# Optimization experiments

Hardware: AMD Instinct MI355X
Metric: run time of the kernel (lower is better)

The kernel has to match this reference:

```python
import jax, jax.numpy as jnp
import numpy as np

B, S, D, H = 4, 2048, 1024, 16
DH = D // H  # 64


def setup_inputs() -> dict:
    key = jax.random.key(0)
    ks = jax.random.split(key, 9)
    scale = 1.0 / np.sqrt(D)
    x = jax.random.normal(ks[0], (B, S, D), dtype=jnp.float32)
    # Stacked per-head projection weights, equivalent to ModuleList of Linear(D, DH)
    Wq = jax.random.uniform(ks[1], (H, D, DH), jnp.float32, -scale, scale)
    bq = jax.random.uniform(ks[2], (H, DH), jnp.float32, -scale, scale)
    Wk = jax.random.uniform(ks[3], (H, D, DH), jnp.float32, -scale, scale)
    bk = jax.random.uniform(ks[4], (H, DH), jnp.float32, -scale, scale)
    Wv = jax.random.uniform(ks[5], (H, D, DH), jnp.float32, -scale, scale)
    bv = jax.random.uniform(ks[6], (H, DH), jnp.float32, -scale, scale)
    Wo = jax.random.uniform(ks[7], (D, D), jnp.float32, -scale, scale)
    bo = jax.random.uniform(ks[8], (D,), jnp.float32, -scale, scale)
    return {"x": x, "Wq": Wq, "bq": bq, "Wk": Wk, "bk": bk,
            "Wv": Wv, "bv": bv, "Wo": Wo, "bo": bo}


def reference(x, Wq, bq, Wk, bk, Wv, bv, Wo, bo):
    # Per-head Linear projections, batched across heads: [B,S,D]x[H,D,DH] -> [B,H,S,DH]
    q = jnp.einsum('bsd,hde->bhse', x, Wq) + bq[None, :, None, :]
    k = jnp.einsum('bsd,hde->bhse', x, Wk) + bk[None, :, None, :]
    v = jnp.einsum('bsd,hde->bhse', x, Wv) + bv[None, :, None, :]
    # Scaled dot-product attention (no mask is applied in the original forward)
    scores = jnp.einsum('bhse,bhte->bhst', q, k) / jnp.sqrt(jnp.float32(DH))
    attn = jax.nn.softmax(scores, axis=-1)
    z = jnp.einsum('bhst,bhte->bhse', attn, v)  # [B,H,S,DH]
    # Concat heads on last dim (head-major order matches torch.cat over dim=-1)
    multihead = jnp.transpose(z, (0, 2, 1, 3)).reshape(B, S, D)
    return multihead @ Wo + bo
```

## Files before the change

### kernel.cpp

```cpp
#include <hip/hip_runtime.h>
#include <hip/hip_bf16.h>
#include <cstdint>
#include <cstddef>


typedef unsigned short u16;
typedef unsigned int u32;
typedef __attribute__((ext_vector_type(8))) __bf16 bf16x8;
typedef __attribute__((ext_vector_type(8))) unsigned short u16x8;
typedef __attribute__((ext_vector_type(4))) float f32x4;
typedef __attribute__((ext_vector_type(4))) unsigned int u32x4;

__device__ __forceinline__ u16 f2bf(float f) {
  union { __hip_bfloat16 h; u16 u; } c;
  c.h = __float2bfloat16(f);
  return c.u;
}
#if defined(__has_builtin)
#if __has_builtin(__builtin_amdgcn_cvt_pk_bf16_f32)
#define HAS_PK_BF16 1
#endif
#endif
__device__ __forceinline__ u32 pk2c(float a, float b) {
#ifdef HAS_PK_BF16
  return __builtin_bit_cast(u32, __builtin_amdgcn_cvt_pk_bf16_f32(a, b));
#else
  const u32 ua = __float_as_uint(a);
  const u32 ub = __float_as_uint(b);
  const u32 ra = ua + 0x7FFFu + ((ua >> 16) & 1u);
  const u32 rb = ub + 0x7FFFu + ((ub >> 16) & 1u);
  return (ra >> 16) | (rb & 0xFFFF0000u);
#endif
}
__device__ __forceinline__ float ex2(float x) {
  return __builtin_amdgcn_exp2f(x);
}

__device__ __forceinline__ void async16(const void* g, void* l) {
  __builtin_amdgcn_global_load_lds(
      (const __attribute__((address_space(1))) void*)g,
      (__attribute__((address_space(3))) void*)l, 16, 0, 0);
}

__global__ void k_pack_all(const float* __restrict__ x,
                           const float* __restrict__ Wq, const float* __restrict__ Wk,
                           const float* __restrict__ Wv,
                           const float* __restrict__ bq, const float* __restrict__ bk,
                           const float* __restrict__ bv,
                           const float* __restrict__ Wo,
                           u16* __restrict__ xb, u16* __restrict__ Wt,
                           float* __restrict__ bqkv, u16* __restrict__ Wot) {
  __shared__ __align__(16) u16 tile[64][72];
  const int bid = blockIdx.x;
  const int t = threadIdx.x;
  if (bid < 1024) {
    const float* src;
    u16* dstp;
    int rstride, n_base, d0;
    if (bid < 768) {
      const int proj = bid >> 8, h = (bid >> 4) & 15, dt = bid & 15;
      const float* Wp = (proj == 0) ? Wq : ((proj == 1) ? Wk : Wv);
      src = Wp + h * 65536 + (dt * 64) * 64;
      rstride = 64;
      n_base = proj * 1024 + h * 64;
      d0 = dt * 64;
      dstp = Wt;
    } else {
      const int tb = bid - 768, nt = tb >> 4, dt = tb & 15;
      src = Wo + (size_t)(dt * 64) * 1024 + nt * 64;
      rstride = 1024;
      n_base = nt * 64;
      d0 = dt * 64;
      dstp = Wot;
    }
    {
      const int row = t >> 2, c0 = (t & 3) * 16;
      const float* s = src + row * rstride + c0;
#pragma unroll
      for (int j = 0; j < 4; ++j) {
        const float4 v = *(const float4*)(s + j * 4);
        ushort4 o;
        o.x = f2bf(v.x); o.y = f2bf(v.y); o.z = f2bf(v.z); o.w = f2bf(v.w);
        *(ushort4*)&tile[row][c0 + j * 4] = o;
      }
    }
    __syncthreads();
    {
      const int e = t >> 2, c0 = (t & 3) * 16;
      u16 buf[16];
#pragma unroll
      for (int i = 0; i < 16; ++i) buf[i] = tile[c0 + i][e];
      u16* d = dstp + (size_t)(n_base + e) * 1024 + d0 + c0;
      *(u16x8*)d = *(const u16x8*)&buf[0];
      *(u16x8*)(d + 8) = *(const u16x8*)&buf[8];
    }
  } else if (bid < 9216) {
    const int i = ((bid - 1024) * 256 + t) * 4;
    const float4 v = *(const float4*)(x + i);
    ushort4 o;
    o.x = f2bf(v.x); o.y = f2bf(v.y); o.z = f2bf(v.z); o.w = f2bf(v.w);
    *(ushort4*)(xb + i) = o;
  } else {
    const int n = (bid - 9216) * 256 + t;
    const int proj = n >> 10, rem = n & 1023, h = rem >> 6, e = rem & 63;
    const float* bp = (proj == 0) ? bq : ((proj == 1) ? bk : bv);
    bqkv[n] = bp[h * 64 + e];
  }
}

template <int MODE>
__global__ __launch_bounds__(256)
void k_gemm(const u16* __restrict__ A, const u16* __restrict__ Bt,
            const float* __restrict__ bias, void* __restrict__ Cout, int ldc) {
  __shared__ __align__(16) u16 Alds[128 * 32];
  __shared__ __align__(16) u16 Blds[128 * 32];
  const int t = threadIdx.x;
  const int lane = t & 63;
  const int w = t >> 6;
  const int l15 = lane & 15;
  const int quad = lane >> 4;
  const int wm = w >> 1, wn = w & 1;
  const int m0 = blockIdx.y << 7;
  const int n0 = blockIdx.x << 7;

  const u16* ga0 = A + (size_t)(m0 + (t >> 2)) * 1024 + (t & 3) * 8;
  const u16* ga1 = ga0 + (size_t)64 * 1024;
  const u16* gb0 = Bt + (size_t)(n0 + (t >> 2)) * 1024 + (t & 3) * 8;
  const u16* gb1 = gb0 + (size_t)64 * 1024;
  u16* const lA0 = Alds + w * 512;
  u16* const lA1 = Alds + w * 512 + 2048;
  u16* const lB0 = Blds + w * 512;
  u16* const lB1 = Blds + w * 512 + 2048;

  f32x4 acc[4][4];
#pragma unroll
  for (int mi = 0; mi < 4; ++mi)
#pragma unroll
    for (int ni = 0; ni < 4; ++ni) acc[mi][ni] = (f32x4){0.f, 0.f, 0.f, 0.f};

  for (int k0 = 0; k0 < 1024; k0 += 32) {
    __syncthreads();
    async16(ga0, lA0); async16(ga1, lA1);
    async16(gb0, lB0); async16(gb1, lB1);
    ga0 += 32; ga1 += 32; gb0 += 32; gb1 += 32;
    __syncthreads();
    bf16x8 af[4], bfr[4];
#pragma unroll
    for (int i = 0; i < 4; ++i) {
      af[i]  = *(const bf16x8*)(Alds + (wm * 64 + i * 16 + l15) * 32 + quad * 8);
      bfr[i] = *(const bf16x8*)(Blds + (wn * 64 + i * 16 + l15) * 32 + quad * 8);
    }
#pragma unroll
    for (int mi = 0; mi < 4; ++mi)
#pragma unroll
      for (int ni = 0; ni < 4; ++ni)
        acc[mi][ni] = __builtin_amdgcn_mfma_f32_16x16x32_bf16(af[mi], bfr[ni], acc[mi][ni], 0, 0, 0);
  }

  const int row0 = m0 + wm * 64;
  const int col0 = n0 + wn * 64;
  const float qscale = (MODE == 0 && col0 < 1024) ? 0.125f * 1.4426950408889634f : 1.0f;
#pragma unroll
  for (int mi = 0; mi < 4; ++mi) {
#pragma unroll
    for (int ni = 0; ni < 4; ++ni) {
      const int col = col0 + ni * 16 + l15;
      const float bb = bias[col];
#pragma unroll
      for (int r = 0; r < 4; ++r) {
        const int row = row0 + mi * 16 + quad * 4 + r;
        const float v = (acc[mi][ni][r] + bb) * qscale;
        if (MODE == 0) ((u16*)Cout)[(size_t)row * ldc + col] = f2bf(v);
        else           ((float*)Cout)[(size_t)row * ldc + col] = v;
      }
    }
  }
}

__global__ __launch_bounds__(256)
void k_vt(const u16* __restrict__ qkv, u16* __restrict__ vtg) {
  __shared__ u16 tile[64][72];
  const int t = threadIdx.x;
  const int bh = blockIdx.y, b = bh >> 4, h = bh & 15;
  const int s0 = blockIdx.x << 6;
  {
    const int row = t >> 2, col0 = (t & 3) * 16;
    const u16* src = qkv + (size_t)(b * 2048 + s0 + row) * 3072 + 2048 + h * 64 + col0;
    const u16x8 v0 = *(const u16x8*)src;
    const u16x8 v1 = *(const u16x8*)(src + 8);
    *(u16x8*)&tile[row][col0] = v0;
    *(u16x8*)&tile[row][col0 + 8] = v1;
  }
  __syncthreads();
  {
    const int e = t >> 2, sc = (t & 3) * 16;
    u16 buf[16];
#pragma unroll
    for (int i = 0; i < 16; ++i) buf[i] = tile[sc + i][e];
    u16* dst = vtg + ((size_t)bh * 64 + e) * 2048 + s0 + sc;
    *(u16x8*)dst = *(const u16x8*)&buf[0];
    *(u16x8*)(dst + 8) = *(const u16x8*)&buf[8];
  }
}

__global__ __launch_bounds__(256)
void k_attn(const u16* __restrict__ qkv, const u16* __restrict__ vtg,
            u16* __restrict__ mh) {
  __shared__ __align__(16) u16 smem[16384];
  u16* const Klds = smem;
  u16* const Vlds = smem + 8192;

  const int t = threadIdx.x;
  const int lane = t & 63;
  const int w = t >> 6;
  const int l15 = lane & 15;
  const int quad = lane >> 4;
  const int bh = blockIdx.x, b = bh >> 4, h = bh & 15;
  const int s0 = blockIdx.y << 7;

  const int lam0 = t >> 3;
  const int key0 = (lam0 & 3) | (((lam0 >> 2) & 3) << 3) | (((lam0 >> 4) & 1) << 2);
  const int ck = (t & 7) ^ (lam0 & 7);
  const u16* kbase = qkv + (size_t)(b * 2048 + key0) * 3072 + 1024 + h * 64 + ck * 8;
  const int e0 = t >> 4;
  const int cv = (t & 15) ^ e0;
  const u16* vbase = vtg + ((size_t)bh * 64 + e0) * 2048 + cv * 8;
  u16* const KldsW = Klds + w * 512;
  u16* const VldsW = Vlds + w * 512;

  bf16x8 aq[2][2];
#pragma unroll
  for (int g = 0; g < 2; ++g)
#pragma unroll
    for (int ks2 = 0; ks2 < 2; ++ks2)
      aq[g][ks2] = *(const bf16x8*)(qkv +
          (size_t)(b * 2048 + s0 + w * 32 + g * 16 + l15) * 3072 +
          h * 64 + ks2 * 32 + quad * 8);

  const u32x4 onesu = (u32x4){0x3F803F80u, 0x3F803F80u, 0x3F803F80u, 0x3F803F80u};
  const bf16x8 ones = __builtin_bit_cast(bf16x8, onesu);

  f32x4 o[2][4];
  f32x4 lacc[2];
#pragma unroll
  for (int g = 0; g < 2; ++g) {
    lacc[g] = (f32x4){0.f, 0.f, 0.f, 0.f};
#pragma unroll
    for (int ne = 0; ne < 4; ++ne) o[g][ne] = (f32x4){0.f, 0.f, 0.f, 0.f};
  }

  for (int kt = 0; kt < 16; ++kt) {
    __syncthreads();
#pragma unroll
    for (int r = 0; r < 4; ++r)
      async16(kbase + r * (32 * 3072), KldsW + r * 2048);
#pragma unroll
    for (int r = 0; r < 4; ++r)
      async16(vbase + r * (16 * 2048), VldsW + r * 2048);
    kbase += 128 * 3072;
    vbase += 128;
    __syncthreads();

#pragma unroll
    for (int ks = 0; ks < 4; ++ks) {
      u32x4 pf[2];
#pragma unroll
      for (int h2 = 0; h2 < 2; ++h2) {
        const int kt8 = ks * 2 + h2;
        const int row = kt8 * 16 + l15;
        const bf16x8 kf0 = *(const bf16x8*)(Klds + row * 64 + ((quad) ^ (l15 & 7)) * 8);
        const bf16x8 kf1 = *(const bf16x8*)(Klds + row * 64 + ((4 + quad) ^ (l15 & 7)) * 8);
        f32x4 st[2];
#pragma unroll
        for (int g = 0; g < 2; ++g) {
          st[g] = __builtin_amdgcn_mfma_f32_16x16x32_bf16(kf0, aq[g][0], (f32x4){0.f,0.f,0.f,0.f}, 0, 0, 0);
          st[g] = __builtin_amdgcn_mfma_f32_16x16x32_bf16(kf1, aq[g][1], st[g], 0, 0, 0);
        }
#pragma unroll
        for (int g = 0; g < 2; ++g) {
          const float p0 = ex2(st[g][0]), p1 = ex2(st[g][1]);
          const float p2 = ex2(st[g][2]), p3 = ex2(st[g][3]);
          pf[g][h2 * 2 + 0] = pk2c(p0, p1);
          pf[g][h2 * 2 + 1] = pk2c(p2, p3);
        }
      }
#pragma unroll
      for (int ne = 0; ne < 4; ++ne) {
        const int e = ne * 16 + l15;
        const bf16x8 bv8 = *(const bf16x8*)(Vlds + e * 128 + (((ks * 4 + quad) ^ l15) & 15) * 8);
#pragma unroll
        for (int g = 0; g < 2; ++g)
          o[g][ne] = __builtin_amdgcn_mfma_f32_16x16x32_bf16(
              __builtin_bit_cast(bf16x8, pf[g]), bv8, o[g][ne], 0, 0, 0);
      }
#pragma unroll
      for (int g = 0; g < 2; ++g)
        lacc[g] = __builtin_amdgcn_mfma_f32_16x16x32_bf16(
            __builtin_bit_cast(bf16x8, pf[g]), ones, lacc[g], 0, 0, 0);
    }
  }

#pragma unroll
  for (int g = 0; g < 2; ++g) {
#pragma unroll
    for (int r = 0; r < 4; ++r) {
      const float iv = 1.f / lacc[g][r];
      const int row = s0 + w * 32 + g * 16 + quad * 4 + r;
#pragma unroll
      for (int ne = 0; ne < 4; ++ne) {
        const int col = h * 64 + ne * 16 + l15;
        mh[(size_t)(b * 2048 + row) * 1024 + col] = f2bf(o[g][ne][r] * iv);
      }
    }
  }
}

extern "C" void kernel_launch(void* const* d_in, const int* in_sizes, int n_in,
                              void* d_out, int out_size, void* d_ws, size_t ws_size,
                              hipStream_t stream) {
  (void)in_sizes; (void)n_in; (void)out_size; (void)ws_size;
  const float* x  = (const float*)d_in[0];
  const float* Wq = (const float*)d_in[1];
  const float* bq = (const float*)d_in[2];
  const float* Wk = (const float*)d_in[3];
  const float* bk = (const float*)d_in[4];
  const float* Wv = (const float*)d_in[5];
  const float* bv = (const float*)d_in[6];
  const float* Wo = (const float*)d_in[7];
  const float* bo = (const float*)d_in[8];

  char* ws = (char*)d_ws;
  u16*   Xb   = (u16*)  (ws + 0);
  u16*   Vtg  = (u16*)  (ws + 0);
  u16*   Wt   = (u16*)  (ws + 16777216);
  float* bqkv = (float*)(ws + 23068672);
  u16*   Wot  = (u16*)  (ws + 23080960);
  u16*   QKV  = (u16*)  (ws + 25178112);
  u16*   MH   = (u16*)  (ws + 75509760);
  float* out  = (float*)d_out;

  k_pack_all <<<9228, 256, 0, stream>>>(x, Wq, Wk, Wv, bq, bk, bv, Wo,
                                        Xb, Wt, bqkv, Wot);
  k_gemm<0>  <<<dim3(24, 64), 256, 0, stream>>>(Xb, Wt, bqkv, (void*)QKV, 3072);
  k_vt       <<<dim3(32, 64), 256, 0, stream>>>(QKV, Vtg);
  k_attn     <<<dim3(64, 16), 256, 0, stream>>>(QKV, Vtg, MH);
  k_gemm<1>  <<<dim3(8, 64), 256, 0, stream>>>(MH, Wot, bo, (void*)out, 1024);
}
```

Baseline: 295.5 us.

## Double-buffer K/V tiles in LDS with async prefetch and MFMA priority hints

Splits the 128-key tile into 64-key tiles and alternates between two LDS buffers, so the next tile's asynchronous global-to-LDS loads are issued before the current tile is computed. A partial vmcnt wait and raw barriers replace the full syncthreads pair. s_setprio is raised around MFMA blocks to favour matrix issue across waves. The V LDS layout and swizzle are changed to match the 64-key stride. The tradeoff is more barriers per key and reliance on the vmcnt count being correct.

```diff
diff --git a/kernel.cpp b/kernel.cpp
--- a/kernel.cpp
+++ b/kernel.cpp
@@ -207,8 +207,6 @@
 void k_attn(const u16* __restrict__ qkv, const u16* __restrict__ vtg,
             u16* __restrict__ mh) {
   __shared__ __align__(16) u16 smem[16384];
-  u16* const Klds = smem;
-  u16* const Vlds = smem + 8192;
 
   const int t = threadIdx.x;
   const int lane = t & 63;
@@ -222,11 +220,12 @@
   const int key0 = (lam0 & 3) | (((lam0 >> 2) & 3) << 3) | (((lam0 >> 4) & 1) << 2);
   const int ck = (t & 7) ^ (lam0 & 7);
   const u16* kbase = qkv + (size_t)(b * 2048 + key0) * 3072 + 1024 + h * 64 + ck * 8;
-  const int e0 = t >> 4;
-  const int cv = (t & 15) ^ e0;
+  const int e0 = t >> 3;
+  const int cv = (t & 7) ^ (e0 & 7);
   const u16* vbase = vtg + ((size_t)bh * 64 + e0) * 2048 + cv * 8;
-  u16* const KldsW = Klds + w * 512;
-  u16* const VldsW = Vlds + w * 512;
+
+  const int kofs = w * 512;
+  const int vofs = 4096 + w * 512;
 
   bf16x8 aq[2][2];
 #pragma unroll
@@ -249,33 +248,49 @@
     for (int ne = 0; ne < 4; ++ne) o[g][ne] = (f32x4){0.f, 0.f, 0.f, 0.f};
   }
 
-  for (int kt = 0; kt < 16; ++kt) {
-    __syncthreads();
-#pragma unroll
-    for (int r = 0; r < 4; ++r)
-      async16(kbase + r * (32 * 3072), KldsW + r * 2048);
-#pragma unroll
-    for (int r = 0; r < 4; ++r)
-      async16(vbase + r * (16 * 2048), VldsW + r * 2048);
-    kbase += 128 * 3072;
-    vbase += 128;
-    __syncthreads();
-
-#pragma unroll
-    for (int ks = 0; ks < 4; ++ks) {
+#pragma unroll
+  for (int r = 0; r < 2; ++r) {
+    async16(kbase + (size_t)r * (32 * 3072), smem + kofs + r * 2048);
+    async16(vbase + (size_t)r * (32 * 2048), smem + vofs + r * 2048);
+  }
+  kbase += 64 * 3072;
+  vbase += 64;
+
+#pragma unroll 2
+  for (int kt = 0; kt < 32; ++kt) {
+    const int cur = kt & 1;
+    const u16* const Kc = smem + cur * 8192;
+    const u16* const Vc = Kc + 4096;
+    u16* const nb = smem + (cur ^ 1) * 8192;
+
+    __builtin_amdgcn_s_barrier();
+#pragma unroll
+    for (int r = 0; r < 2; ++r) {
+      async16(kbase + (size_t)r * (32 * 3072), nb + kofs + r * 2048);
+      async16(vbase + (size_t)r * (32 * 2048), nb + vofs + r * 2048);
+    }
+    kbase += 64 * 3072;
+    vbase += 64;
+    asm volatile("s_waitcnt vmcnt(4)" ::: "memory");
+    __builtin_amdgcn_s_barrier();
+    __builtin_amdgcn_sched_barrier(0);
+
+#pragma unroll
+    for (int ks = 0; ks < 2; ++ks) {
       u32x4 pf[2];
 #pragma unroll
       for (int h2 = 0; h2 < 2; ++h2) {
-        const int kt8 = ks * 2 + h2;
-        const int row = kt8 * 16 + l15;
-        const bf16x8 kf0 = *(const bf16x8*)(Klds + row * 64 + ((quad) ^ (l15 & 7)) * 8);
-        const bf16x8 kf1 = *(const bf16x8*)(Klds + row * 64 + ((4 + quad) ^ (l15 & 7)) * 8);
+        const int row = (ks * 2 + h2) * 16 + l15;
+        const bf16x8 kf0 = *(const bf16x8*)(Kc + row * 64 + ((quad) ^ (l15 & 7)) * 8);
+        const bf16x8 kf1 = *(const bf16x8*)(Kc + row * 64 + ((4 + quad) ^ (l15 & 7)) * 8);
         f32x4 st[2];
+        __builtin_amdgcn_s_setprio(1);
 #pragma unroll
         for (int g = 0; g < 2; ++g) {
           st[g] = __builtin_amdgcn_mfma_f32_16x16x32_bf16(kf0, aq[g][0], (f32x4){0.f,0.f,0.f,0.f}, 0, 0, 0);
           st[g] = __builtin_amdgcn_mfma_f32_16x16x32_bf16(kf1, aq[g][1], st[g], 0, 0, 0);
         }
+        __builtin_amdgcn_s_setprio(0);
 #pragma unroll
         for (int g = 0; g < 2; ++g) {
           const float p0 = ex2(st[g][0]), p1 = ex2(st[g][1]);
@@ -284,10 +299,11 @@
           pf[g][h2 * 2 + 1] = pk2c(p2, p3);
         }
       }
+      __builtin_amdgcn_s_setprio(1);
 #pragma unroll
       for (int ne = 0; ne < 4; ++ne) {
         const int e = ne * 16 + l15;
-        const bf16x8 bv8 = *(const bf16x8*)(Vlds + e * 128 + (((ks * 4 + quad) ^ l15) & 15) * 8);
+        const bf16x8 bv8 = *(const bf16x8*)(Vc + e * 64 + ((ks * 4 + quad) ^ (e & 7)) * 8);
 #pragma unroll
         for (int g = 0; g < 2; ++g)
           o[g][ne] = __builtin_amdgcn_mfma_f32_16x16x32_bf16(
@@ -297,6 +313,7 @@
       for (int g = 0; g < 2; ++g)
         lacc[g] = __builtin_amdgcn_mfma_f32_16x16x32_bf16(
             __builtin_bit_cast(bf16x8, pf[g]), ones, lacc[g], 0, 0, 0);
+      __builtin_amdgcn_s_setprio(0);
     }
   }
 
```

Measured after the change: 296.7 us. No clear change (+0.4%).
